# Optimization experiments

Hardware: AMD Instinct MI355X
Metric: run time of the kernel (lower is better)

## Reference

```python
import jax, jax.numpy as jnp
import numpy as np

HEAD_DIM = 128
SCALE = HEAD_DIM ** -0.5  # head_scaling == up_scaling == 1/sqrt(head_dim)


def setup_inputs() -> dict:
    key = jax.random.key(0)
    kq, kk, ku, kv = jax.random.split(key, 4)
    B, H, S, D = 2, 16, 2048, 128
    Hk, I = 4, 2048
    Q = jax.random.normal(kq, (B, H, S, D), dtype=jnp.float32)
    K = jax.random.normal(kk, (Hk, I, D), dtype=jnp.float32)
    U = jax.random.normal(ku, (Hk, I, D), dtype=jnp.float32)
    V = jax.random.normal(kv, (Hk, I, D), dtype=jnp.float32)
    return {"Q": Q, "K": K, "U": U, "V": V}


def reference(Q, K, U, V):
    # Q: (B, H, S, D); K/U/V: (Hk, I, D); GQA grouping G = H // Hk
    B, H, S, D = Q.shape
    Hk, I, _ = K.shape
    G = H // Hk
    Qr = Q.reshape(B, Hk, G, S, D)
    # gate scores and up projection, both scaled by 1/sqrt(D)
    M = jnp.einsum('bkgsd,kid->bkgsi', Qr, K) * SCALE
    N = jnp.einsum('bkgsd,kid->bkgsi', Qr, U) * SCALE
    A = jax.nn.silu(M) * N  # gated activation, (B, Hk, G, S, I)
    out = jnp.einsum('bkgsi,kid->bkgsd', A, V)
    return out.reshape(B, H, S, D)
```

## Files before the change

kernel.cpp:

```cpp
#include <hip/hip_runtime.h>

#define B_   2
#define H_   16
#define G_   4
#define S_   2048
#define D_   128
#define I_   2048

#define BM   256
#define BN   64
#define TPB  512
#define NIT  (I_ / BN)

#define LDA  40

#define KUSZ (BN * 128)
#define VSZ  (D_ * 64)

#define KIDX(r,c) ((r)*128 + ((c) ^ (((r)&7)<<3)))
#define VIDX(d,c) ((d)*64  + ((c) ^ (((d)&7)<<3)))

static constexpr float SCALE = 0.08838834764831845f;

typedef __fp16   p2v __attribute__((ext_vector_type(2)));
typedef _Float16 h8v __attribute__((ext_vector_type(8)));
typedef float    f4v __attribute__((ext_vector_type(4)));

__global__ __launch_bounds__(TPB, 2) void flashmlp_kernel(
    const float* __restrict__ Qg, const float* __restrict__ Kg,
    const float* __restrict__ Ug, const float* __restrict__ Vg,
    float* __restrict__ Og)
{
    __shared__ _Float16 Ks[2 * KUSZ];
    __shared__ _Float16 Us[2 * KUSZ];
    __shared__ _Float16 Vt[2 * VSZ];
    __shared__ _Float16 As[BM * LDA];

    const int bid   = blockIdx.x;
    const int xcd   = bid & 7;
    const int kh    = xcd >> 1;
    const int j     = ((bid >> 3) << 1) | (xcd & 1);
    const int stile = j & 7;
    const int bg    = j >> 3;
    const int b     = bg >> 2;
    const int g     = bg & 3;
    const int h     = kh * G_ + g;

    const int tid  = threadIdx.x;
    const int wave = tid >> 6;
    const int lane = tid & 63;
    const int m16  = lane & 15;
    const int qq   = lane >> 4;

    const size_t qbase  = ((size_t)(b * H_ + h) * S_ + (size_t)stile * BM) * D_;
    const size_t kvbase = (size_t)kh * I_ * D_;

    h8v qf[2][4];
#pragma unroll
    for (int rt = 0; rt < 2; ++rt) {
        const float* qp = Qg + qbase + (size_t)(wave * 32 + rt * 16 + m16) * D_;
#pragma unroll
        for (int ks = 0; ks < 4; ++ks) {
            const float4 a = *(const float4*)(qp + ks * 32 + qq * 8);
            const float4 c = *(const float4*)(qp + ks * 32 + qq * 8 + 4);
            h8v v;
            p2v* v2 = (p2v*)&v;
            v2[0] = __builtin_amdgcn_cvt_pkrtz(a.x * SCALE, a.y * SCALE);
            v2[1] = __builtin_amdgcn_cvt_pkrtz(a.z * SCALE, a.w * SCALE);
            v2[2] = __builtin_amdgcn_cvt_pkrtz(c.x * SCALE, c.y * SCALE);
            v2[3] = __builtin_amdgcn_cvt_pkrtz(c.z * SCALE, c.w * SCALE);
            qf[rt][ks] = v;
        }
    }

    f4v acc_o[2][8];
#pragma unroll
    for (int rt = 0; rt < 2; ++rt)
#pragma unroll
        for (int dt = 0; dt < 8; ++dt)
            acc_o[rt][dt] = f4v{0.f, 0.f, 0.f, 0.f};

    const int sr  = tid >> 3;
    const int sc  = (tid & 7) * 16;
    const int d0  = tid & 127;
    const int io4 = (tid >> 7) * 16;
    const float* kbp = Kg + kvbase + (size_t)sr * D_ + sc;
    const float* ubp = Ug + kvbase + (size_t)sr * D_ + sc;

    float4 kpre[4], upre[4];
    float  vpre[16];

#pragma unroll
    for (int g4 = 0; g4 < 4; ++g4) {
        kpre[g4] = *(const float4*)(kbp + g4 * 4);
        upre[g4] = *(const float4*)(ubp + g4 * 4);
    }
#pragma unroll
    for (int jj = 0; jj < 16; ++jj)
        vpre[jj] = Vg[kvbase + (size_t)(io4 + jj) * D_ + d0];
    {
        h8v kb[2], ub[2], vb[2];
        p2v* kb2 = (p2v*)kb; p2v* ub2 = (p2v*)ub; p2v* vb2 = (p2v*)vb;
#pragma unroll
        for (int g4 = 0; g4 < 4; ++g4) {
            kb2[2 * g4 + 0] = __builtin_amdgcn_cvt_pkrtz(kpre[g4].x, kpre[g4].y);
            kb2[2 * g4 + 1] = __builtin_amdgcn_cvt_pkrtz(kpre[g4].z, kpre[g4].w);
            ub2[2 * g4 + 0] = __builtin_amdgcn_cvt_pkrtz(upre[g4].x, upre[g4].y);
            ub2[2 * g4 + 1] = __builtin_amdgcn_cvt_pkrtz(upre[g4].z, upre[g4].w);
        }
#pragma unroll
        for (int jj = 0; jj < 8; ++jj)
            vb2[jj] = __builtin_amdgcn_cvt_pkrtz(vpre[2 * jj], vpre[2 * jj + 1]);
        *(h8v*)(&Ks[KIDX(sr, sc + 0)]) = kb[0];
        *(h8v*)(&Ks[KIDX(sr, sc + 8)]) = kb[1];
        *(h8v*)(&Us[KIDX(sr, sc + 0)]) = ub[0];
        *(h8v*)(&Us[KIDX(sr, sc + 8)]) = ub[1];
        *(h8v*)(&Vt[VIDX(d0, io4 + 0)]) = vb[0];
        *(h8v*)(&Vt[VIDX(d0, io4 + 8)]) = vb[1];
    }
    __syncthreads();

    for (int it = 0; it < NIT; ++it) {
        const int cur = it & 1;
        const _Float16* ksb = Ks + cur * KUSZ;
        const _Float16* usb = Us + cur * KUSZ;
        const _Float16* vtb = Vt + cur * VSZ;

        const bool more = (it + 1 < NIT);
        if (more) {
            const float* kp = kbp + (size_t)(it + 1) * BN * D_;
            const float* up = ubp + (size_t)(it + 1) * BN * D_;
#pragma unroll
            for (int g4 = 0; g4 < 4; ++g4) {
                kpre[g4] = *(const float4*)(kp + g4 * 4);
                upre[g4] = *(const float4*)(up + g4 * 4);
            }
            const float* vp = Vg + kvbase + (size_t)((it + 1) * BN + io4) * D_ + d0;
#pragma unroll
            for (int jj = 0; jj < 16; ++jj)
                vpre[jj] = vp[(size_t)jj * D_];
        }

        _Float16 ag[2][4][4];
#pragma unroll
        for (int ct = 0; ct < 4; ++ct) {
            f4v am[2], an[2];
            am[0] = f4v{0.f, 0.f, 0.f, 0.f}; am[1] = am[0];
            an[0] = am[0]; an[1] = am[0];
            __builtin_amdgcn_s_setprio(1);
#pragma unroll
            for (int ks = 0; ks < 4; ++ks) {
                const h8v kf = *(const h8v*)(&ksb[KIDX(ct * 16 + m16, ks * 32 + qq * 8)]);
                const h8v uf = *(const h8v*)(&usb[KIDX(ct * 16 + m16, ks * 32 + qq * 8)]);
                am[0] = __builtin_amdgcn_mfma_f32_16x16x32_f16(qf[0][ks], kf, am[0], 0, 0, 0);
                am[1] = __builtin_amdgcn_mfma_f32_16x16x32_f16(qf[1][ks], kf, am[1], 0, 0, 0);
                an[0] = __builtin_amdgcn_mfma_f32_16x16x32_f16(qf[0][ks], uf, an[0], 0, 0, 0);
                an[1] = __builtin_amdgcn_mfma_f32_16x16x32_f16(qf[1][ks], uf, an[1], 0, 0, 0);
            }
            __builtin_amdgcn_s_setprio(0);
#pragma unroll
            for (int rt = 0; rt < 2; ++rt)
#pragma unroll
                for (int r = 0; r < 4; ++r) {
                    const float mv = am[rt][r];
                    const float nv = an[rt][r];
                    const float sg = __builtin_amdgcn_rcpf(1.f + __expf(-mv));
                    ag[rt][ct][r] = (_Float16)(mv * sg * nv);
                }
        }

        if (more) {
            _Float16* ksn = Ks + (cur ^ 1) * KUSZ;
            _Float16* usn = Us + (cur ^ 1) * KUSZ;
            _Float16* vtn = Vt + (cur ^ 1) * VSZ;
            h8v kb[2], ub[2], vb[2];
            p2v* kb2 = (p2v*)kb; p2v* ub2 = (p2v*)ub; p2v* vb2 = (p2v*)vb;
#pragma unroll
            for (int g4 = 0; g4 < 4; ++g4) {
                kb2[2 * g4 + 0] = __builtin_amdgcn_cvt_pkrtz(kpre[g4].x, kpre[g4].y);
                kb2[2 * g4 + 1] = __builtin_amdgcn_cvt_pkrtz(kpre[g4].z, kpre[g4].w);
                ub2[2 * g4 + 0] = __builtin_amdgcn_cvt_pkrtz(upre[g4].x, upre[g4].y);
                ub2[2 * g4 + 1] = __builtin_amdgcn_cvt_pkrtz(upre[g4].z, upre[g4].w);
            }
#pragma unroll
            for (int jj = 0; jj < 8; ++jj)
                vb2[jj] = __builtin_amdgcn_cvt_pkrtz(vpre[2 * jj], vpre[2 * jj + 1]);
            *(h8v*)(&ksn[KIDX(sr, sc + 0)]) = kb[0];
            *(h8v*)(&ksn[KIDX(sr, sc + 8)]) = kb[1];
            *(h8v*)(&usn[KIDX(sr, sc + 0)]) = ub[0];
            *(h8v*)(&usn[KIDX(sr, sc + 8)]) = ub[1];
            *(h8v*)(&vtn[VIDX(d0, io4 + 0)]) = vb[0];
            *(h8v*)(&vtn[VIDX(d0, io4 + 8)]) = vb[1];
        }

#pragma unroll
        for (int hh = 0; hh < 2; ++hh) {
#pragma unroll
            for (int c2 = 0; c2 < 2; ++c2) {
                const int ct = hh * 2 + c2;
#pragma unroll
                for (int rt = 0; rt < 2; ++rt)
#pragma unroll
                    for (int r = 0; r < 4; ++r)
                        As[(wave * 32 + rt * 16 + qq * 4 + r) * LDA + c2 * 16 + m16] = ag[rt][ct][r];
            }
            h8v vfr[8];
#pragma unroll
            for (int dt = 0; dt < 8; ++dt)
                vfr[dt] = *(const h8v*)(&vtb[VIDX(dt * 16 + m16, hh * 32 + qq * 8)]);
#pragma unroll
            for (int rt = 0; rt < 2; ++rt) {
                const h8v af = *(const h8v*)(&As[(wave * 32 + rt * 16 + m16) * LDA + qq * 8]);
                __builtin_amdgcn_s_setprio(1);
#pragma unroll
                for (int dt = 0; dt < 8; ++dt)
                    acc_o[rt][dt] = __builtin_amdgcn_mfma_f32_16x16x32_f16(af, vfr[dt], acc_o[rt][dt], 0, 0, 0);
                __builtin_amdgcn_s_setprio(0);
            }
        }

        __syncthreads();
    }

#pragma unroll
    for (int rt = 0; rt < 2; ++rt) {
#pragma unroll
        for (int r = 0; r < 4; ++r) {
            const int row = stile * BM + wave * 32 + rt * 16 + qq * 4 + r;
            float* op = Og + ((size_t)(b * H_ + h) * S_ + row) * D_;
#pragma unroll
            for (int dt = 0; dt < 8; ++dt)
                op[dt * 16 + m16] = acc_o[rt][dt][r];
        }
    }
}

extern "C" void kernel_launch(void* const* d_in, const int* in_sizes, int n_in,
                              void* d_out, int out_size, void* d_ws, size_t ws_size,
                              hipStream_t stream) {
    const float* Q = (const float*)d_in[0];
    const float* K = (const float*)d_in[1];
    const float* U = (const float*)d_in[2];
    const float* V = (const float*)d_in[3];
    float* out = (float*)d_out;

    const int grid = (S_ / BM) * B_ * H_;
    flashmlp_kernel<<<dim3(grid), dim3(TPB), 0, stream>>>(Q, K, U, V, out);
}
```

Measured before the change: 208.4 us.

## Switch to 32x32x16 MFMA with transposed products and register-resident gated activations

```diff
diff --git a/kernel.cpp b/kernel.cpp
--- a/kernel.cpp
+++ b/kernel.cpp
@@ -12,8 +12,6 @@
 #define TPB  512
 #define NIT  (I_ / BN)
 
-#define LDA  40
-
 #define KUSZ (BN * 128)
 #define VSZ  (D_ * 64)
 
@@ -22,9 +20,16 @@
 
 static constexpr float SCALE = 0.08838834764831845f;
 
-typedef __fp16   p2v __attribute__((ext_vector_type(2)));
-typedef _Float16 h8v __attribute__((ext_vector_type(8)));
-typedef float    f4v __attribute__((ext_vector_type(4)));
+typedef __fp16   p2v  __attribute__((ext_vector_type(2)));
+typedef _Float16 h8v  __attribute__((ext_vector_type(8)));
+typedef float    f4v  __attribute__((ext_vector_type(4)));
+typedef float    f16v __attribute__((ext_vector_type(16)));
+typedef int      i4v  __attribute__((ext_vector_type(4)));
+
+__device__ __forceinline__ int pkf16(float a, float b) {
+    p2v t = __builtin_amdgcn_cvt_pkrtz(a, b);
+    int r; __builtin_memcpy(&r, &t, 4); return r;
+}
 
 __global__ __launch_bounds__(TPB, 2) void flashmlp_kernel(
     const float* __restrict__ Qg, const float* __restrict__ Kg,
@@ -34,7 +39,6 @@
     __shared__ _Float16 Ks[2 * KUSZ];
     __shared__ _Float16 Us[2 * KUSZ];
     __shared__ _Float16 Vt[2 * VSZ];
-    __shared__ _Float16 As[BM * LDA];
 
     const int bid   = blockIdx.x;
     const int xcd   = bid & 7;
@@ -49,36 +53,35 @@
     const int tid  = threadIdx.x;
     const int wave = tid >> 6;
     const int lane = tid & 63;
-    const int m16  = lane & 15;
-    const int qq   = lane >> 4;
+    const int l31  = lane & 31;
+    const int hl   = lane >> 5;
 
     const size_t qbase  = ((size_t)(b * H_ + h) * S_ + (size_t)stile * BM) * D_;
     const size_t kvbase = (size_t)kh * I_ * D_;
 
-    h8v qf[2][4];
-#pragma unroll
-    for (int rt = 0; rt < 2; ++rt) {
-        const float* qp = Qg + qbase + (size_t)(wave * 32 + rt * 16 + m16) * D_;
-#pragma unroll
-        for (int ks = 0; ks < 4; ++ks) {
-            const float4 a = *(const float4*)(qp + ks * 32 + qq * 8);
-            const float4 c = *(const float4*)(qp + ks * 32 + qq * 8 + 4);
+    h8v qf[8];
+    {
+        const float* qp = Qg + qbase + (size_t)(wave * 32 + l31) * D_;
+#pragma unroll
+        for (int ks = 0; ks < 8; ++ks) {
+            const float4 a = *(const float4*)(qp + ks * 16 + hl * 8);
+            const float4 c = *(const float4*)(qp + ks * 16 + hl * 8 + 4);
             h8v v;
             p2v* v2 = (p2v*)&v;
             v2[0] = __builtin_amdgcn_cvt_pkrtz(a.x * SCALE, a.y * SCALE);
             v2[1] = __builtin_amdgcn_cvt_pkrtz(a.z * SCALE, a.w * SCALE);
             v2[2] = __builtin_amdgcn_cvt_pkrtz(c.x * SCALE, c.y * SCALE);
             v2[3] = __builtin_amdgcn_cvt_pkrtz(c.z * SCALE, c.w * SCALE);
-            qf[rt][ks] = v;
-        }
-    }
-
-    f4v acc_o[2][8];
-#pragma unroll
-    for (int rt = 0; rt < 2; ++rt)
-#pragma unroll
-        for (int dt = 0; dt < 8; ++dt)
-            acc_o[rt][dt] = f4v{0.f, 0.f, 0.f, 0.f};
+            qf[ks] = v;
+        }
+    }
+
+    f16v acc_o[4];
+#pragma unroll
+    for (int dt = 0; dt < 4; ++dt)
+#pragma unroll
+        for (int e = 0; e < 16; ++e)
+            acc_o[dt][e] = 0.f;
 
     const int sr  = tid >> 3;
     const int sc  = (tid & 7) * 16;
@@ -141,32 +144,41 @@
                 vpre[jj] = vp[(size_t)jj * D_];
         }
 
-        _Float16 ag[2][4][4];
-#pragma unroll
-        for (int ct = 0; ct < 4; ++ct) {
-            f4v am[2], an[2];
-            am[0] = f4v{0.f, 0.f, 0.f, 0.f}; am[1] = am[0];
-            an[0] = am[0]; an[1] = am[0];
+        h8v pb[4];
+#pragma unroll
+        for (int t2 = 0; t2 < 2; ++t2) {
+            f16v am, an;
+#pragma unroll
+            for (int e = 0; e < 16; ++e) { am[e] = 0.f; an[e] = 0.f; }
             __builtin_amdgcn_s_setprio(1);
 #pragma unroll
-            for (int ks = 0; ks < 4; ++ks) {
-                const h8v kf = *(const h8v*)(&ksb[KIDX(ct * 16 + m16, ks * 32 + qq * 8)]);
-                const h8v uf = *(const h8v*)(&usb[KIDX(ct * 16 + m16, ks * 32 + qq * 8)]);
-                am[0] = __builtin_amdgcn_mfma_f32_16x16x32_f16(qf[0][ks], kf, am[0], 0, 0, 0);
-                am[1] = __builtin_amdgcn_mfma_f32_16x16x32_f16(qf[1][ks], kf, am[1], 0, 0, 0);
-                an[0] = __builtin_amdgcn_mfma_f32_16x16x32_f16(qf[0][ks], uf, an[0], 0, 0, 0);
-                an[1] = __builtin_amdgcn_mfma_f32_16x16x32_f16(qf[1][ks], uf, an[1], 0, 0, 0);
+            for (int ks = 0; ks < 8; ++ks) {
+                const h8v kf = *(const h8v*)(&ksb[KIDX(t2 * 32 + l31, ks * 16 + hl * 8)]);
+                const h8v uf = *(const h8v*)(&usb[KIDX(t2 * 32 + l31, ks * 16 + hl * 8)]);
+                am = __builtin_amdgcn_mfma_f32_32x32x16_f16(kf, qf[ks], am, 0, 0, 0);
+                an = __builtin_amdgcn_mfma_f32_32x32x16_f16(uf, qf[ks], an, 0, 0, 0);
             }
             __builtin_amdgcn_s_setprio(0);
-#pragma unroll
-            for (int rt = 0; rt < 2; ++rt)
-#pragma unroll
-                for (int r = 0; r < 4; ++r) {
-                    const float mv = am[rt][r];
-                    const float nv = an[rt][r];
-                    const float sg = __builtin_amdgcn_rcpf(1.f + __expf(-mv));
-                    ag[rt][ct][r] = (_Float16)(mv * sg * nv);
-                }
+
+            int P[8];
+#pragma unroll
+            for (int p = 0; p < 8; ++p) {
+                const float m0 = am[2 * p + 0], n0 = an[2 * p + 0];
+                const float m1 = am[2 * p + 1], n1 = an[2 * p + 1];
+                const float g0 = m0 * __builtin_amdgcn_rcpf(1.f + __expf(-m0)) * n0;
+                const float g1 = m1 * __builtin_amdgcn_rcpf(1.f + __expf(-m1)) * n1;
+                P[p] = pkf16(g0, g1);
+            }
+            auto sA = __builtin_amdgcn_permlane32_swap(P[0], P[2], false, false);
+            auto sB = __builtin_amdgcn_permlane32_swap(P[1], P[3], false, false);
+            auto sC = __builtin_amdgcn_permlane32_swap(P[4], P[6], false, false);
+            auto sD = __builtin_amdgcn_permlane32_swap(P[5], P[7], false, false);
+            i4v wlo = i4v{static_cast<int>(sA[0]), static_cast<int>(sB[0]),
+                          static_cast<int>(sA[1]), static_cast<int>(sB[1])};
+            i4v whi = i4v{static_cast<int>(sC[0]), static_cast<int>(sD[0]),
+                          static_cast<int>(sC[1]), static_cast<int>(sD[1])};
+            __builtin_memcpy(&pb[2 * t2 + 0], &wlo, 16);
+            __builtin_memcpy(&pb[2 * t2 + 1], &whi, 16);
         }
 
         if (more) {
@@ -194,44 +206,32 @@
         }
 
 #pragma unroll
-        for (int hh = 0; hh < 2; ++hh) {
-#pragma unroll
-            for (int c2 = 0; c2 < 2; ++c2) {
-                const int ct = hh * 2 + c2;
-#pragma unroll
-                for (int rt = 0; rt < 2; ++rt)
-#pragma unroll
-                    for (int r = 0; r < 4; ++r)
-                        As[(wave * 32 + rt * 16 + qq * 4 + r) * LDA + c2 * 16 + m16] = ag[rt][ct][r];
-            }
-            h8v vfr[8];
-#pragma unroll
-            for (int dt = 0; dt < 8; ++dt)
-                vfr[dt] = *(const h8v*)(&vtb[VIDX(dt * 16 + m16, hh * 32 + qq * 8)]);
-#pragma unroll
-            for (int rt = 0; rt < 2; ++rt) {
-                const h8v af = *(const h8v*)(&As[(wave * 32 + rt * 16 + m16) * LDA + qq * 8]);
-                __builtin_amdgcn_s_setprio(1);
-#pragma unroll
-                for (int dt = 0; dt < 8; ++dt)
-                    acc_o[rt][dt] = __builtin_amdgcn_mfma_f32_16x16x32_f16(af, vfr[dt], acc_o[rt][dt], 0, 0, 0);
-                __builtin_amdgcn_s_setprio(0);
-            }
+        for (int ks2 = 0; ks2 < 4; ++ks2) {
+            h8v va[4];
+#pragma unroll
+            for (int dt = 0; dt < 4; ++dt)
+                va[dt] = *(const h8v*)(&vtb[VIDX(dt * 32 + l31, ks2 * 16 + hl * 8)]);
+            __builtin_amdgcn_s_setprio(1);
+#pragma unroll
+            for (int dt = 0; dt < 4; ++dt)
+                acc_o[dt] = __builtin_amdgcn_mfma_f32_32x32x16_f16(va[dt], pb[ks2], acc_o[dt], 0, 0, 0);
+            __builtin_amdgcn_s_setprio(0);
         }
 
         __syncthreads();
     }
 
-#pragma unroll
-    for (int rt = 0; rt < 2; ++rt) {
-#pragma unroll
-        for (int r = 0; r < 4; ++r) {
-            const int row = stile * BM + wave * 32 + rt * 16 + qq * 4 + r;
-            float* op = Og + ((size_t)(b * H_ + h) * S_ + row) * D_;
-#pragma unroll
-            for (int dt = 0; dt < 8; ++dt)
-                op[dt * 16 + m16] = acc_o[rt][dt][r];
-        }
+    {
+        const int qrow = stile * BM + wave * 32 + l31;
+        float* op = Og + ((size_t)(b * H_ + h) * S_ + qrow) * D_;
+#pragma unroll
+        for (int dt = 0; dt < 4; ++dt)
+#pragma unroll
+            for (int g4 = 0; g4 < 4; ++g4) {
+                f4v v = f4v{acc_o[dt][4 * g4 + 0], acc_o[dt][4 * g4 + 1],
+                            acc_o[dt][4 * g4 + 2], acc_o[dt][4 * g4 + 3]};
+                *(f4v*)(op + dt * 32 + g4 * 8 + hl * 4) = v;
+            }
     }
 }
 
```

Result: faster. 200.3 us (-3.9%).
